# Optimization experiments

Hardware: AMD Instinct MI355X
Metric: run time of the kernel (lower is better)

Reference implementation:

```python
import jax, jax.numpy as jnp
import numpy as np

B, D, O = 8192, 192, 16  # batch, input_dim==grid_size, output_dim


def setup_inputs() -> dict:
    key = jax.random.key(0)
    k1, k2 = jax.random.split(key)
    x = jax.random.uniform(k1, (B, D), dtype=jnp.float32)          # [B, D]
    splines = jax.random.normal(k2, (O, D, D), dtype=jnp.float32) * 0.05  # [O, grid, in]
    grid = jnp.linspace(0.0, 1.0, D, dtype=jnp.float32)            # [G] == [D]
    return {"x": x, "splines": splines, "grid": grid}


def reference(x, splines, grid):
    # Hat basis: basis[n, g, d] = relu(1 - |x[n, d] - grid[g]|)
    basis = jnp.maximum(0.0, 1.0 - jnp.abs(x[:, None, :] - grid[None, :, None]))  # [B, G, D]
    # out[n, i] = sum_{g, d} splines[i, g, d] * basis[n, g, d]
    return jnp.einsum("bgd,ogd->bo", basis, splines)  # [B, O]
```

## Files before the change

kernel.cpp:

```cpp
#include <hip/hip_runtime.h>
#include <hip/hip_bf16.h>


#define Dn 192
#define Gn 192
#define On 16
#define Bn 8192

__device__ __forceinline__ unsigned short f2bf(float f) {
    union { float f; unsigned u; } v; v.f = f;
    unsigned r = v.u + 0x7FFF + ((v.u >> 16) & 1);
    return (unsigned short)(r >> 16);
}

__global__ __launch_bounds__(256) void kan_pre(const float* __restrict__ sp,
                                               const float* __restrict__ grid,
                                               unsigned* __restrict__ tab) {
    int gtid = blockIdx.x * blockDim.x + threadIdx.x;
    int w = gtid >> 6;
    int lane = threadIdx.x & 63;
    if (w >= Dn * On) return;
    int d = w >> 4;
    int i = w & 15;

    int g0 = lane * 3;
    const float* s_base = sp + (size_t)i * Gn * Dn + d;
    float s0 = s_base[(size_t)(g0 + 0) * Dn];
    float s1 = s_base[(size_t)(g0 + 1) * Dn];
    float s2 = s_base[(size_t)(g0 + 2) * Dn];
    float q0 = s0 * grid[g0 + 0];
    float q1 = s1 * grid[g0 + 1];
    float q2 = s2 * grid[g0 + 2];

    float lp1 = s0 + s1, lp2 = lp1 + s2;
    float lq1 = q0 + q1, lq2 = lq1 + q2;
    float sP = lp2, sQ = lq2;
    #pragma unroll
    for (int off = 1; off < 64; off <<= 1) {
        float pP = __shfl_up(sP, off);
        float pQ = __shfl_up(sQ, off);
        if (lane >= off) { sP += pP; sQ += pQ; }
    }
    float exP = sP - lp2, exQ = sQ - lq2;
    float T = __shfl(sP, 63);
    float U = __shfl(sQ, 63);

    float P[3] = { exP + s0, exP + lp1, exP + lp2 };
    float Q[3] = { exQ + q0, exQ + lq1, exQ + lq2 };

    #pragma unroll
    for (int k = 0; k < 3; ++k) {
        int g = g0 + k;
        float A  = 2.0f * P[k] - T;
        float Cp = T - U + 2.0f * Q[k];
        unsigned packed = (unsigned)f2bf(A) | ((unsigned)f2bf(Cp) << 16);
        tab[((size_t)d * Gn + g) * On + i] = packed;
    }
}

#define QD (Dn / 4)
#define WPB 4

__global__ __launch_bounds__(256) void kan_main(const float* __restrict__ x,
                                                const unsigned* __restrict__ tab,
                                                float* __restrict__ out) {
    int t = threadIdx.x;
    int lane = t & 63;
    int w = t >> 6;
    int n = blockIdx.x * WPB + w;
    int i = lane & 15;
    int q = lane >> 4;

    const float4* xr = (const float4*)(x + (size_t)n * Dn + q * QD);
    const unsigned* tb = tab + (size_t)q * QD * Gn * On + i;

    float acc = 0.0f;
    #pragma unroll
    for (int d4 = 0; d4 < QD / 4; ++d4) {
        float4 xv = xr[d4];
        float vx[4] = { xv.x, xv.y, xv.z, xv.w };
        #pragma unroll
        for (int k = 0; k < 4; ++k) {
            float v = vx[k];
            int g = (int)(v * 191.0f);
            g = (g < 0) ? 0 : (g > 191 ? 191 : g);
            unsigned e = tb[((d4 * 4 + k) * Gn + g) * On];
            union { unsigned u; float f; } A, C;
            A.u = e << 16;
            C.u = e & 0xFFFF0000u;
            acc += C.f;
            acc = fmaf(-v, A.f, acc);
        }
    }
    acc += __shfl_xor(acc, 16);
    acc += __shfl_xor(acc, 32);
    if (lane < 16) out[(size_t)n * On + i] = acc;
}

__global__ __launch_bounds__(256) void kan_naive(const float* __restrict__ x,
                                                 const float* __restrict__ sp,
                                                 const float* __restrict__ grid,
                                                 float* __restrict__ out) {
    __shared__ float xs[Dn];
    __shared__ float gsh[Gn];
    __shared__ float red[4];
    int n = blockIdx.x;
    int t = threadIdx.x;
    if (t < Dn) { xs[t] = x[(size_t)n * Dn + t]; gsh[t] = grid[t]; }
    __syncthreads();
    float acc[On];
    #pragma unroll
    for (int i = 0; i < On; ++i) acc[i] = 0.0f;
    for (int idx = t; idx < Gn * Dn; idx += 256) {
        int g = idx / Dn;
        int d = idx - g * Dn;
        float b = fmaxf(0.0f, 1.0f - fabsf(xs[d] - gsh[g]));
        #pragma unroll
        for (int i = 0; i < On; ++i)
            acc[i] += sp[(size_t)i * Gn * Dn + idx] * b;
    }
    for (int i = 0; i < On; ++i) {
        float v = acc[i];
        #pragma unroll
        for (int off = 32; off > 0; off >>= 1) v += __shfl_down(v, off);
        if ((t & 63) == 0) red[t >> 6] = v;
        __syncthreads();
        if (t == 0) out[(size_t)n * On + i] = red[0] + red[1] + red[2] + red[3];
        __syncthreads();
    }
}

extern "C" void kernel_launch(void* const* d_in, const int* in_sizes, int n_in,
                              void* d_out, int out_size, void* d_ws, size_t ws_size,
                              hipStream_t stream) {
    const float* x    = (const float*)d_in[0];
    const float* sp   = (const float*)d_in[1];
    const float* grid = (const float*)d_in[2];
    float* out = (float*)d_out;

    const size_t TAB_BYTES = (size_t)Dn * Gn * On * sizeof(unsigned);
    if (ws_size >= TAB_BYTES) {
        unsigned* tab = (unsigned*)d_ws;
        kan_pre<<<(Dn * On * 64 + 255) / 256, 256, 0, stream>>>(sp, grid, tab);
        kan_main<<<Bn / WPB, 256, 0, stream>>>(x, tab, out);
    } else {
        kan_naive<<<Bn, 256, 0, stream>>>(x, sp, grid, out);
    }
}
```

Before: 24.73 us.

## Stage per-chunk lookup table in LDS and split input dim across blocks

The main kernel is replaced by one that splits the input dimension into 16 chunks. Each block copies its chunk's 12-row table slice (144KB) into LDS and then serves 512 batch rows from it, so table gathers hit LDS instead of global/L2 memory. Per-chunk partial sums go to a workspace buffer and are summed by a new reduction kernel. The cost is an extra launch, 8MB of partial-sum writes and reads, a grid of only 256 large blocks with one block per CU because of LDS size, and a larger workspace requirement.

```diff
diff --git a/kernel.cpp b/kernel.cpp
--- a/kernel.cpp
+++ b/kernel.cpp
@@ -6,6 +6,13 @@
 #define Gn 192
 #define On 16
 #define Bn 8192
+
+#define CHUNKS 16
+#define CD (Dn / CHUNKS)
+#define NBLK 16
+#define NPB (Bn / NBLK)
+#define TPB 1024
+#define SLICE (CD * Gn * On)
 
 __device__ __forceinline__ unsigned short f2bf(float f) {
     union { float f; unsigned u; } v; v.f = f;
@@ -58,43 +65,60 @@
     }
 }
 
-#define QD (Dn / 4)
-#define WPB 4
+__global__ __launch_bounds__(TPB) void kan_main_lds(const float* __restrict__ x,
+                                                    const unsigned* __restrict__ tab,
+                                                    float* __restrict__ partial) {
+    __shared__ unsigned lds[SLICE];
+    int t  = threadIdx.x;
+    int nb = blockIdx.x;
+    int c  = blockIdx.y;
 
-__global__ __launch_bounds__(256) void kan_main(const float* __restrict__ x,
-                                                const unsigned* __restrict__ tab,
-                                                float* __restrict__ out) {
-    int t = threadIdx.x;
-    int lane = t & 63;
-    int w = t >> 6;
-    int n = blockIdx.x * WPB + w;
-    int i = lane & 15;
-    int q = lane >> 4;
+    const uint4* src = (const uint4*)(tab + (size_t)c * SLICE);
+    uint4* dst = (uint4*)lds;
+    #pragma unroll
+    for (int j = 0; j < SLICE / 4 / TPB; ++j)
+        dst[t + j * TPB] = src[t + j * TPB];
+    __syncthreads();
 
-    const float4* xr = (const float4*)(x + (size_t)n * Dn + q * QD);
-    const unsigned* tb = tab + (size_t)q * QD * Gn * On + i;
+    int i    = t & 15;
+    int nsub = t >> 4;
+    int d0   = c * CD;
+    float* pout = partial + (size_t)c * Bn * On;
 
-    float acc = 0.0f;
     #pragma unroll
-    for (int d4 = 0; d4 < QD / 4; ++d4) {
-        float4 xv = xr[d4];
-        float vx[4] = { xv.x, xv.y, xv.z, xv.w };
+    for (int k = 0; k < NPB / 64; ++k) {
+        int n = nb * NPB + nsub + 64 * k;
+        const float4* xr = (const float4*)(x + (size_t)n * Dn + d0);
+        float acc = 0.0f;
         #pragma unroll
-        for (int k = 0; k < 4; ++k) {
-            float v = vx[k];
-            int g = (int)(v * 191.0f);
-            g = (g < 0) ? 0 : (g > 191 ? 191 : g);
-            unsigned e = tb[((d4 * 4 + k) * Gn + g) * On];
-            union { unsigned u; float f; } A, C;
-            A.u = e << 16;
-            C.u = e & 0xFFFF0000u;
-            acc += C.f;
-            acc = fmaf(-v, A.f, acc);
+        for (int d4 = 0; d4 < CD / 4; ++d4) {
+            float4 xv = xr[d4];
+            float vx[4] = { xv.x, xv.y, xv.z, xv.w };
+            #pragma unroll
+            for (int kk = 0; kk < 4; ++kk) {
+                float v = vx[kk];
+                int g = (int)(v * 191.0f);
+                g = (g < 0) ? 0 : (g > 191 ? 191 : g);
+                unsigned e = lds[((d4 * 4 + kk) * Gn + g) * On + i];
+                union { unsigned u; float f; } A, C;
+                A.u = e << 16;
+                C.u = e & 0xFFFF0000u;
+                acc += C.f;
+                acc = fmaf(-v, A.f, acc);
+            }
         }
+        pout[(size_t)n * On + i] = acc;
     }
-    acc += __shfl_xor(acc, 16);
-    acc += __shfl_xor(acc, 32);
-    if (lane < 16) out[(size_t)n * On + i] = acc;
+}
+
+__global__ __launch_bounds__(256) void kan_reduce(const float* __restrict__ partial,
+                                                  float* __restrict__ out) {
+    int j = blockIdx.x * 256 + threadIdx.x;
+    float s = 0.0f;
+    #pragma unroll
+    for (int c = 0; c < CHUNKS; ++c)
+        s += partial[(size_t)c * Bn * On + j];
+    out[j] = s;
 }
 
 __global__ __launch_bounds__(256) void kan_naive(const float* __restrict__ x,
@@ -138,11 +162,14 @@
     const float* grid = (const float*)d_in[2];
     float* out = (float*)d_out;
 
-    const size_t TAB_BYTES = (size_t)Dn * Gn * On * sizeof(unsigned);
-    if (ws_size >= TAB_BYTES) {
-        unsigned* tab = (unsigned*)d_ws;
+    const size_t TAB_BYTES  = (size_t)Dn * Gn * On * sizeof(unsigned);
+    const size_t PART_BYTES = (size_t)CHUNKS * Bn * On * sizeof(float);
+    if (ws_size >= TAB_BYTES + PART_BYTES) {
+        unsigned* tab   = (unsigned*)d_ws;
+        float* partial  = (float*)((char*)d_ws + TAB_BYTES);
         kan_pre<<<(Dn * On * 64 + 255) / 256, 256, 0, stream>>>(sp, grid, tab);
-        kan_main<<<Bn / WPB, 256, 0, stream>>>(x, tab, out);
+        kan_main_lds<<<dim3(NBLK, CHUNKS), TPB, 0, stream>>>(x, tab, partial);
+        kan_reduce<<<Bn * On / 256, 256, 0, stream>>>(partial, out);
     } else {
         kan_naive<<<Bn, 256, 0, stream>>>(x, sp, grid, out);
     }
```

After: 29.94 us. +21.1%, slower.
